# Performance work log

Measured on AMD Instinct MI355X. Metric: run time of the kernel, lower is better.

Reference implementation:

```python
import jax, jax.numpy as jnp
import numpy as np
import math
from jax import lax

B, L, C_IN = 32, 1024, 21
D_MODEL, N_HEADS, D_FF = 512, 8, 2048
E_LAYERS, FACTOR, MA_K = 3, 1, 25
N_CLASSES = 10
EPS = 1e-5


def setup_inputs() -> dict:
    key = jax.random.key(0)
    ks = jax.random.split(key, 12)
    s = 0.02
    return {
        "x_enc": jax.random.normal(ks[0], (B, L, C_IN), jnp.float32),
        "x_mark_enc": jnp.ones((B, L), jnp.float32),
        "conv_emb_w": jax.random.normal(ks[1], (D_MODEL, C_IN, 3), jnp.float32) * s,
        "Wq": jax.random.normal(ks[2], (E_LAYERS, D_MODEL, D_MODEL), jnp.float32) * s,
        "bq": jnp.zeros((E_LAYERS, D_MODEL), jnp.float32),
        "Wk": jax.random.normal(ks[3], (E_LAYERS, D_MODEL, D_MODEL), jnp.float32) * s,
        "bk": jnp.zeros((E_LAYERS, D_MODEL), jnp.float32),
        "Wv": jax.random.normal(ks[4], (E_LAYERS, D_MODEL, D_MODEL), jnp.float32) * s,
        "bv": jnp.zeros((E_LAYERS, D_MODEL), jnp.float32),
        "Wo": jax.random.normal(ks[5], (E_LAYERS, D_MODEL, D_MODEL), jnp.float32) * s,
        "bo": jnp.zeros((E_LAYERS, D_MODEL), jnp.float32),
        "Wff1": jax.random.normal(ks[6], (E_LAYERS, D_FF, D_MODEL), jnp.float32) * s,
        "Wff2": jax.random.normal(ks[7], (E_LAYERS, D_MODEL, D_FF), jnp.float32) * s,
        "ln_g": jnp.ones((D_MODEL,), jnp.float32),
        "ln_b": jnp.zeros((D_MODEL,), jnp.float32),
        "Wproj": jax.random.normal(ks[8], (N_CLASSES, D_MODEL * L), jnp.float32) * 0.001,
        "bproj": jnp.zeros((N_CLASSES,), jnp.float32),
    }


def token_embed(x, w):
    # x: [B, L, C] -> Conv1d(C->D, k=3, circular padding, no bias) -> [B, L, D]
    xp = jnp.pad(x.transpose(0, 2, 1), ((0, 0), (0, 0), (1, 1)), mode='wrap')  # [B,C,L+2]
    y = lax.conv_general_dilated(xp, w, (1,), 'VALID', dimension_numbers=('NCH', 'OIH', 'NCH'))
    return y.transpose(0, 2, 1)


def moving_avg(x, k):
    # replicate-pad then avg-pool with stride 1 (kernel k odd -> same length)
    pad = (k - 1) // 2
    xp = jnp.concatenate([jnp.repeat(x[:, :1], pad, 1), x, jnp.repeat(x[:, -1:], pad, 1)], axis=1)
    return lax.reduce_window(xp, 0.0, lax.add, (1, k, 1), (1, 1, 1), 'VALID') / k


def series_decomp(x, k):
    m = moving_avg(x, k)
    return x - m, m


def auto_correlation(q, k, v):
    # q,k,v: [B, L, H, E]; FFT-based period correlation + time-delay aggregation (inference variant)
    B_, L_, H, E = q.shape
    qf = jnp.fft.rfft(q.transpose(0, 2, 3, 1), axis=-1)   # [B,H,E,Lf]
    kf = jnp.fft.rfft(k.transpose(0, 2, 3, 1), axis=-1)
    corr = jnp.fft.irfft(qf * jnp.conj(kf), n=L_, axis=-1)  # [B,H,E,L]
    values = v.transpose(0, 2, 3, 1)                        # [B,H,E,L]
    mean_value = corr.mean(axis=(1, 2))                     # [B,L]
    top_k = int(FACTOR * math.log(L_))
    weights, delay = lax.top_k(mean_value, top_k)           # [B,k]
    tmp_corr = jax.nn.softmax(weights, axis=-1)
    tmp_values = jnp.concatenate([values, values], axis=-1)  # [B,H,E,2L]
    init_index = jnp.arange(L_)
    agg = jnp.zeros_like(values)
    for i in range(top_k):  # small fixed loop (top_k = 6)
        idx = init_index[None, :] + delay[:, i:i + 1]        # [B,L]
        idx_b = jnp.broadcast_to(idx[:, None, None, :], (B_, H, E, L_))
        pat = jnp.take_along_axis(tmp_values, idx_b, axis=-1)
        agg = agg + pat * tmp_corr[:, i][:, None, None, None]
    return agg.transpose(0, 3, 1, 2)  # [B,L,H,E]


def encoder_layer(x, Wq, bq, Wk, bk, Wv, bv, Wo, bo, Wf1, Wf2):
    B_, L_, D = x.shape
    E = D // N_HEADS
    q = (x @ Wq.T + bq).reshape(B_, L_, N_HEADS, E)
    k = (x @ Wk.T + bk).reshape(B_, L_, N_HEADS, E)
    v = (x @ Wv.T + bv).reshape(B_, L_, N_HEADS, E)
    a = auto_correlation(q, k, v).reshape(B_, L_, D)
    a = a @ Wo.T + bo
    x = x + a
    x, _ = series_decomp(x, MA_K)
    y = jax.nn.gelu(jnp.einsum('bld,fd->blf', x, Wf1), approximate=False)
    y = jnp.einsum('blf,df->bld', y, Wf2)
    res, _ = series_decomp(x + y, MA_K)
    return res


def my_layernorm(x, g, b):
    mu = x.mean(-1, keepdims=True)
    var = ((x - mu) ** 2).mean(-1, keepdims=True)
    xh = (x - mu) / jnp.sqrt(var + EPS) * g + b
    return xh - xh.mean(axis=1, keepdims=True)  # special LN: remove seq-wise mean


def reference(x_enc, x_mark_enc, conv_emb_w, Wq, bq, Wk, bk, Wv, bv, Wo, bo, Wff1, Wff2, ln_g, ln_b, Wproj, bproj):
    x = token_embed(x_enc, conv_emb_w)  # DataEmbedding_wo_pos with x_mark=None
    for l in range(E_LAYERS):
        x = encoder_layer(x, Wq[l], bq[l], Wk[l], bk[l], Wv[l], bv[l], Wo[l], bo[l], Wff1[l], Wff2[l])
    x = my_layernorm(x, ln_g, ln_b)
    out = jax.nn.gelu(x, approximate=False)
    out = out * x_mark_enc[:, :, None]
    out = out.reshape(out.shape[0], -1)
    return out @ Wproj.T + bproj
```

## Files before the change

kernel.cpp:

```cpp
#include <hip/hip_runtime.h>
#include <cstdint>


using u16 = unsigned short;
typedef _Float16 f16x8 __attribute__((ext_vector_type(8)));
typedef float f32x4 __attribute__((ext_vector_type(4)));

#define BB 32
#define LL 1024
#define DD 512
#define DFF 2048

__device__ __forceinline__ float bf2f(u16 u) {
  union { uint32_t i; float f; } v; v.i = ((uint32_t)u) << 16; return v.f;
}
__device__ __forceinline__ u16 f2bf(float f) {
  union { float f; uint32_t i; } v; v.f = f;
  uint32_t r = (v.i + 0x7FFFu + ((v.i >> 16) & 1u)) >> 16;
  return (u16)r;
}
__device__ __forceinline__ float ldi(const void* p, long i, int isf) {
  return isf ? ((const float*)p)[i] : bf2f(((const u16*)p)[i]);
}
__device__ __forceinline__ float gelu_f(float x) {
  return 0.5f * x * (1.0f + erff(x * 0.70710678118654752440f));
}
__device__ __forceinline__ void gld16(const void* g, void* l) {
  __builtin_amdgcn_global_load_lds(
      (const __attribute__((address_space(1))) void*)g,
      (__attribute__((address_space(3))) void*)l, 16, 0, 0);
}

union H8 { f16x8 v; uint4 u; _Float16 h[8]; };
union H4 { uint2 u; _Float16 h[4]; };

__global__ void detect_k(const uint32_t* __restrict__ mark, int* __restrict__ FLAG) {
  if (threadIdx.x == 0) FLAG[0] = (mark[0] == 0x3F800000u) ? 1 : 0;
}

__global__ __launch_bounds__(256) void wT_k(const void* __restrict__ w,
                                            float* __restrict__ wT,
                                            const int* __restrict__ FLAG) {
  const int isf = *FLAG;
  int idx = blockIdx.x * 256 + threadIdx.x;
  if (idx >= 63 * DD) return;
  int c3t = idx / DD;
  int d = idx - c3t * DD;
  wT[idx] = ldi(w, (long)d * 63 + c3t, isf);
}

__global__ __launch_bounds__(256) void conv_embed_k(
    const void* __restrict__ xe, const float* __restrict__ wT,
    float* __restrict__ X, _Float16* __restrict__ XH, _Float16* __restrict__ XL,
    const int* __restrict__ FLAG) {
  const int isf = *FLAG;
  int b = blockIdx.y;
  int l0 = blockIdx.x * 16;
  __shared__ float xs[18][21];
  int tid = threadIdx.x;
  for (int i = tid; i < 18 * 21; i += 256) {
    int r = i / 21, c = i % 21;
    int row = (l0 - 1 + r + LL) & (LL - 1);
    xs[r][c] = ldi(xe, ((long)b * LL + row) * 21 + c, isf);
  }
  __syncthreads();
  for (int d = tid; d < DD; d += 256) {
    float acc[16];
#pragma unroll
    for (int ll = 0; ll < 16; ll++) acc[ll] = 0.0f;
    for (int c = 0; c < 21; c++) {
#pragma unroll
      for (int t = 0; t < 3; t++) {
        float wv = wT[(c * 3 + t) * DD + d];
#pragma unroll
        for (int ll = 0; ll < 16; ll++) acc[ll] += wv * xs[t + ll][c];
      }
    }
    for (int ll = 0; ll < 16; ll++) {
      long idx = ((long)b * LL + l0 + ll) * DD + d;
      float v = acc[ll];
      X[idx] = v;
      _Float16 hv = (_Float16)v;
      XH[idx] = hv;
      XL[idx] = (_Float16)((v - (float)hv) * 512.0f);
    }
  }
}

__global__ __launch_bounds__(256) void tsplit2_k(
    const void* __restrict__ W1, const void* __restrict__ W2, long off,
    _Float16* __restrict__ T1H, _Float16* __restrict__ T1L,
    _Float16* __restrict__ T2H, _Float16* __restrict__ T2L,
    const int* __restrict__ FLAG) {
  const int isf = *FLAG;
  const void* W = blockIdx.z ? W2 : W1;
  _Float16* TH = blockIdx.z ? T2H : T1H;
  _Float16* TL = blockIdx.z ? T2L : T1L;
  __shared__ float t[64][65];
  const int f0 = blockIdx.x * 64, m0 = blockIdx.y * 64;
  const int tid = threadIdx.x;
  const int c = tid & 63, rb = tid >> 6;
#pragma unroll
  for (int r = rb; r < 64; r += 4)
    t[r][c] = ldi(W, off + (long)(f0 + r) * DD + m0 + c, isf);
  __syncthreads();
#pragma unroll
  for (int r = rb; r < 64; r += 4) {
    float v = t[c][r];
    long o = (long)(m0 + r) * DD + f0 + c;
    _Float16 hv = (_Float16)v;
    TH[o] = hv;
    TL[o] = (_Float16)((v - (float)hv) * 512.0f);
  }
}

__global__ __launch_bounds__(256) void split_k(const float* __restrict__ src,
                                               _Float16* __restrict__ dh,
                                               _Float16* __restrict__ dl, int n) {
  long i = ((long)blockIdx.x * 256 + threadIdx.x) * 8;
  if (i >= n) return;
  float4 a = *(const float4*)(src + i);
  float4 b = *(const float4*)(src + i + 4);
  float x[8] = {a.x, a.y, a.z, a.w, b.x, b.y, b.z, b.w};
  H8 h, l;
#pragma unroll
  for (int j = 0; j < 8; j++) {
    _Float16 hv = (_Float16)x[j];
    h.h[j] = hv;
    l.h[j] = (_Float16)((x[j] - (float)hv) * 512.0f);
  }
  *(uint4*)(dh + i) = h.u;
  *(uint4*)(dl + i) = l.u;
}

__global__ __launch_bounds__(256) void acvt_k(const float* __restrict__ src,
                                              _Float16* __restrict__ dst, int n) {
  long i = ((long)blockIdx.x * 256 + threadIdx.x) * 8;
  if (i >= n) return;
  float4 a = *(const float4*)(src + i);
  float4 b = *(const float4*)(src + i + 4);
  H8 r;
  r.h[0] = (_Float16)a.x; r.h[1] = (_Float16)a.y;
  r.h[2] = (_Float16)a.z; r.h[3] = (_Float16)a.w;
  r.h[4] = (_Float16)b.x; r.h[5] = (_Float16)b.y;
  r.h[6] = (_Float16)b.z; r.h[7] = (_Float16)b.w;
  *(uint4*)(dst + i) = r.u;
}

__global__ __launch_bounds__(256) void wcvt6_k(
    const void* __restrict__ Wv, const void* __restrict__ Wo,
    const void* __restrict__ W1, const void* __restrict__ W2,
    long oW, long oF,
    _Float16* __restrict__ Wvh, _Float16* __restrict__ Woh,
    _Float16* __restrict__ W1h, _Float16* __restrict__ W2h,
    const int* __restrict__ FLAG) {
  const int isf = *FLAG;
  long e = ((long)blockIdx.x * 256 + threadIdx.x) * 8;
  const void* src; long soff; _Float16* dst;
  if (e < 262144) { src = Wv; soff = oW + e; dst = Wvh + e; }
  else if (e < 524288) { src = Wo; soff = oW + (e - 262144); dst = Woh + (e - 262144); }
  else if (e < 1572864) { src = W1; soff = oF + (e - 524288); dst = W1h + (e - 524288); }
  else { src = W2; soff = oF + (e - 1572864); dst = W2h + (e - 1572864); }
  H8 r;
  if (isf) {
    const float* s = (const float*)src + soff;
    float4 a = *(const float4*)s;
    float4 b = *(const float4*)(s + 4);
    r.h[0] = (_Float16)a.x; r.h[1] = (_Float16)a.y;
    r.h[2] = (_Float16)a.z; r.h[3] = (_Float16)a.w;
    r.h[4] = (_Float16)b.x; r.h[5] = (_Float16)b.y;
    r.h[6] = (_Float16)b.z; r.h[7] = (_Float16)b.w;
  } else {
    const u16* s = (const u16*)src + soff;
    uint4 u = *(const uint4*)s;
    r.h[0] = (_Float16)bf2f((u16)(u.x & 0xffff));
    r.h[1] = (_Float16)bf2f((u16)(u.x >> 16));
    r.h[2] = (_Float16)bf2f((u16)(u.y & 0xffff));
    r.h[3] = (_Float16)bf2f((u16)(u.y >> 16));
    r.h[4] = (_Float16)bf2f((u16)(u.z & 0xffff));
    r.h[5] = (_Float16)bf2f((u16)(u.z >> 16));
    r.h[6] = (_Float16)bf2f((u16)(u.w & 0xffff));
    r.h[7] = (_Float16)bf2f((u16)(u.w >> 16));
  }
  *(uint4*)(dst) = r.u;
}

__global__ __launch_bounds__(256) void gemm_z(
    const _Float16* __restrict__ Ah, const _Float16* __restrict__ Al,
    const _Float16* __restrict__ Bh, const _Float16* __restrict__ Bl,
    _Float16* __restrict__ Zh, _Float16* __restrict__ Zl,
    int M, int N, int K) {
  __shared__ __align__(16) _Float16 AsH[128 * 32];
  __shared__ __align__(16) _Float16 AsL[128 * 32];
  __shared__ __align__(16) _Float16 BsH[128 * 32];
  __shared__ __align__(16) _Float16 BsL[128 * 32];
  const int n0 = blockIdx.x * 128, m0 = blockIdx.y * 128;
  const int tid = threadIdx.x;
  const int lane = tid & 63, wvi = tid >> 6;
  const int wm = (wvi >> 1) * 64, wn = (wvi & 1) * 64;
  const int l15 = lane & 15, quad = lane >> 4;
  const int ib = wvi * 128 + lane;
  const int r0 = ib >> 2, r1 = r0 + 16;
  const int c0 = ((ib & 3) ^ ((r0 >> 1) & 3)) * 8;
  const int c1 = ((ib & 3) ^ ((r1 >> 1) & 3)) * 8;
  const int lb0 = wvi * 1024, lb1 = wvi * 1024 + 512;
  const long ga0 = (long)(m0 + r0) * K + c0;
  const long ga1 = (long)(m0 + r1) * K + c1;
  const long gb0 = (long)(n0 + r0) * K + c0;
  const long gb1 = (long)(n0 + r1) * K + c1;
  f32x4 aM[4][4], aC[4][4];
#pragma unroll
  for (int i = 0; i < 4; i++)
#pragma unroll
    for (int j = 0; j < 4; j++) {
      aM[i][j] = (f32x4){0.f, 0.f, 0.f, 0.f};
      aC[i][j] = (f32x4){0.f, 0.f, 0.f, 0.f};
    }
  for (int k0 = 0; k0 < K; k0 += 32) {
    __syncthreads();
    gld16(Ah + ga0 + k0, AsH + lb0);
    gld16(Ah + ga1 + k0, AsH + lb1);
    gld16(Al + ga0 + k0, AsL + lb0);
    gld16(Al + ga1 + k0, AsL + lb1);
    gld16(Bh + gb0 + k0, BsH + lb0);
    gld16(Bh + gb1 + k0, BsH + lb1);
    gld16(Bl + gb0 + k0, BsL + lb0);
    gld16(Bl + gb1 + k0, BsL + lb1);
    __syncthreads();
    f16x8 fah[4], fal[4], fbh[4], fbl[4];
#pragma unroll
    for (int mi = 0; mi < 4; mi++) {
      int r = wm + mi * 16 + l15;
      int o = r * 32 + ((quad ^ ((r >> 1) & 3)) * 8);
      fah[mi] = *(const f16x8*)&AsH[o];
      fal[mi] = *(const f16x8*)&AsL[o];
    }
#pragma unroll
    for (int ni = 0; ni < 4; ni++) {
      int r = wn + ni * 16 + l15;
      int o = r * 32 + ((quad ^ ((r >> 1) & 3)) * 8);
      fbh[ni] = *(const f16x8*)&BsH[o];
      fbl[ni] = *(const f16x8*)&BsL[o];
    }
#pragma unroll
    for (int mi = 0; mi < 4; mi++)
#pragma unroll
      for (int ni = 0; ni < 4; ni++) {
        aM[mi][ni] = __builtin_amdgcn_mfma_f32_16x16x32_f16(
            fah[mi], fbh[ni], aM[mi][ni], 0, 0, 0);
        aC[mi][ni] = __builtin_amdgcn_mfma_f32_16x16x32_f16(
            fah[mi], fbl[ni], aC[mi][ni], 0, 0, 0);
        aC[mi][ni] = __builtin_amdgcn_mfma_f32_16x16x32_f16(
            fal[mi], fbh[ni], aC[mi][ni], 0, 0, 0);
      }
  }
#pragma unroll
  for (int mi = 0; mi < 4; mi++) {
    int rowg = m0 + wm + mi * 16 + quad * 4;
#pragma unroll
    for (int ni = 0; ni < 4; ni++) {
      int colg = n0 + wn + ni * 16 + l15;
#pragma unroll
      for (int rr = 0; rr < 4; rr++) {
        long off = (long)(rowg + rr) * N + colg;
        float z = aM[mi][ni][rr] + aC[mi][ni][rr] * (1.0f / 512.0f);
        _Float16 zh = (_Float16)z;
        Zh[off] = zh;
        Zl[off] = (_Float16)((z - (float)zh) * 512.0f);
      }
    }
  }
}

__global__ __launch_bounds__(256) void qkmv_hl(
    const _Float16* __restrict__ Zh, const _Float16* __restrict__ Zl,
    const _Float16* __restrict__ Xh, const _Float16* __restrict__ Xl,
    float* __restrict__ MV) {
  __shared__ __align__(16) _Float16 AsH[128 * 32];
  __shared__ __align__(16) _Float16 AsL[128 * 32];
  __shared__ __align__(16) _Float16 BsH[128 * 32];
  __shared__ __align__(16) _Float16 BsL[128 * 32];
  __shared__ float diag[255];
  const int bz = blockIdx.z;
  const long bb = (long)bz * LL * DD;
  const int n0 = blockIdx.x * 128, m0 = blockIdx.y * 128;
  const int tid = threadIdx.x;
  const int lane = tid & 63, wvi = tid >> 6;
  const int wm = (wvi >> 1) * 64, wn = (wvi & 1) * 64;
  const int l15 = lane & 15, quad = lane >> 4;
  const int ib = wvi * 128 + lane;
  const int r0 = ib >> 2, r1 = r0 + 16;
  const int c0 = ((ib & 3) ^ ((r0 >> 1) & 3)) * 8;
  const int c1 = ((ib & 3) ^ ((r1 >> 1) & 3)) * 8;
  const int lb0 = wvi * 1024, lb1 = wvi * 1024 + 512;
  const long ga0 = bb + (long)(m0 + r0) * DD + c0;
  const long ga1 = bb + (long)(m0 + r1) * DD + c1;
  const long gb0 = bb + (long)(n0 + r0) * DD + c0;
  const long gb1 = bb + (long)(n0 + r1) * DD + c1;
  if (tid < 255) diag[tid] = 0.0f;
  f32x4 aM[4][4], aC[4][4];
#pragma unroll
  for (int i = 0; i < 4; i++)
#pragma unroll
    for (int j = 0; j < 4; j++) {
      aM[i][j] = (f32x4){0.f, 0.f, 0.f, 0.f};
      aC[i][j] = (f32x4){0.f, 0.f, 0.f, 0.f};
    }
  for (int k0 = 0; k0 < DD; k0 += 32) {
    __syncthreads();
    gld16(Zh + ga0 + k0, AsH + lb0);
    gld16(Zh + ga1 + k0, AsH + lb1);
    gld16(Zl + ga0 + k0, AsL + lb0);
    gld16(Zl + ga1 + k0, AsL + lb1);
    gld16(Xh + gb0 + k0, BsH + lb0);
    gld16(Xh + gb1 + k0, BsH + lb1);
    gld16(Xl + gb0 + k0, BsL + lb0);
    gld16(Xl + gb1 + k0, BsL + lb1);
    __syncthreads();
    f16x8 fah[4], fal[4], fbh[4], fbl[4];
#pragma unroll
    for (int mi = 0; mi < 4; mi++) {
      int r = wm + mi * 16 + l15;
      int o = r * 32 + ((quad ^ ((r >> 1) & 3)) * 8);
      fah[mi] = *(const f16x8*)&AsH[o];
      fal[mi] = *(const f16x8*)&AsL[o];
    }
#pragma unroll
    for (int ni = 0; ni < 4; ni++) {
      int r = wn + ni * 16 + l15;
      int o = r * 32 + ((quad ^ ((r >> 1) & 3)) * 8);
      fbh[ni] = *(const f16x8*)&BsH[o];
      fbl[ni] = *(const f16x8*)&BsL[o];
    }
#pragma unroll
    for (int mi = 0; mi < 4; mi++)
#pragma unroll
      for (int ni = 0; ni < 4; ni++) {
        aM[mi][ni] = __builtin_amdgcn_mfma_f32_16x16x32_f16(
            fah[mi], fbh[ni], aM[mi][ni], 0, 0, 0);
        aC[mi][ni] = __builtin_amdgcn_mfma_f32_16x16x32_f16(
            fah[mi], fbl[ni], aC[mi][ni], 0, 0, 0);
        aC[mi][ni] = __builtin_amdgcn_mfma_f32_16x16x32_f16(
            fal[mi], fbh[ni], aC[mi][ni], 0, 0, 0);
      }
  }
#pragma unroll
  for (int g = -3; g <= 3; g++) {
#pragma unroll
    for (int rr = 0; rr < 4; rr++) {
      float s = 0.0f;
#pragma unroll
      for (int mi = 0; mi < 4; mi++) {
        int ni = mi - g;
        if (ni >= 0 && ni < 4)
          s += aM[mi][ni][rr] + aC[mi][ni][rr] * (1.0f / 512.0f);
      }
      int d = 127 + (wm - wn) + g * 16 + quad * 4 + rr - l15;
      atomicAdd(&diag[d], s);
    }
  }
  __syncthreads();
  if (tid < 255) {
    int tau = (m0 - n0 + tid - 127 + LL) & (LL - 1);
    atomicAdd(&MV[(long)bz * LL + tau], diag[tid] * (1.0f / 512.0f));
  }
}

template <int FLAGS>
__global__ __launch_bounds__(256) void gemm_h(
    const _Float16* __restrict__ A, const _Float16* __restrict__ W,
    const void* __restrict__ biasBase, long bOff,
    const float* __restrict__ R, void* __restrict__ Cout,
    int M, int N, int K, const int* __restrict__ FLAG) {
  constexpr bool HAS_BIAS = (FLAGS & 1) != 0;
  constexpr bool DO_GELU = (FLAGS & 2) != 0;
  constexpr bool DO_RES = (FLAGS & 4) != 0;
  constexpr bool OUT_H = (FLAGS & 8) != 0;
  __shared__ __align__(16) _Float16 As[128 * 64];
  __shared__ __align__(16) _Float16 Bs[128 * 64];
  const int n0 = blockIdx.x * 128, m0 = blockIdx.y * 128;
  const int tid = threadIdx.x;
  const int lane = tid & 63, wvi = tid >> 6;
  const int wm = (wvi >> 1) * 64, wn = (wvi & 1) * 64;
  const int l15 = lane & 15, quad = lane >> 4;
  const _Float16* gA[4];
  const _Float16* gB[4];
  int ldsOff[4];
#pragma unroll
  for (int j = 0; j < 4; j++) {
    int ib = wvi * 256 + j * 64 + lane;
    int row = ib >> 3, p = ib & 7;
    int gc = ((p & 4) | ((p & 3) ^ ((row >> 1) & 3))) * 8;
    gA[j] = A + (long)(m0 + row) * K + gc;
    gB[j] = W + (long)(n0 + row) * K + gc;
    ldsOff[j] = wvi * 2048 + j * 512;
  }
  f32x4 acc[4][4];
#pragma unroll
  for (int i = 0; i < 4; i++)
#pragma unroll
    for (int j = 0; j < 4; j++) acc[i][j] = (f32x4){0.f, 0.f, 0.f, 0.f};
  for (int k0 = 0; k0 < K; k0 += 64) {
    __syncthreads();
#pragma unroll
    for (int j = 0; j < 4; j++) gld16(gA[j] + k0, As + ldsOff[j]);
#pragma unroll
    for (int j = 0; j < 4; j++) gld16(gB[j] + k0, Bs + ldsOff[j]);
    __syncthreads();
#pragma unroll
    for (int ks = 0; ks < 2; ks++) {
      f16x8 af[4], bfr[4];
#pragma unroll
      for (int mi = 0; mi < 4; mi++) {
        int r = wm + mi * 16 + l15;
        af[mi] = *(const f16x8*)&As[r * 64 + (ks * 4 + (quad ^ ((r >> 1) & 3))) * 8];
      }
#pragma unroll
      for (int ni = 0; ni < 4; ni++) {
        int r = wn + ni * 16 + l15;
        bfr[ni] = *(const f16x8*)&Bs[r * 64 + (ks * 4 + (quad ^ ((r >> 1) & 3))) * 8];
      }
#pragma unroll
      for (int mi = 0; mi < 4; mi++)
#pragma unroll
        for (int ni = 0; ni < 4; ni++)
          acc[mi][ni] = __builtin_amdgcn_mfma_f32_16x16x32_f16(
              af[mi], bfr[ni], acc[mi][ni], 0, 0, 0);
    }
  }
  float bcol[4];
  if constexpr (HAS_BIAS) {
    const int isf = *FLAG;
#pragma unroll
    for (int ni = 0; ni < 4; ni++)
      bcol[ni] = ldi(biasBase, bOff + n0 + wn + ni * 16 + l15, isf);
  }
#pragma unroll
  for (int mi = 0; mi < 4; mi++) {
    int rowg = m0 + wm + mi * 16 + quad * 4;
#pragma unroll
    for (int ni = 0; ni < 4; ni++) {
      int colg = n0 + wn + ni * 16 + l15;
#pragma unroll
      for (int rr = 0; rr < 4; rr++) {
        long off = (long)(rowg + rr) * N + colg;
        float v = acc[mi][ni][rr];
        if constexpr (HAS_BIAS) v += bcol[ni];
        if constexpr (DO_RES) v += R[off];
        if constexpr (DO_GELU) v = gelu_f(v);
        if constexpr (OUT_H) ((_Float16*)Cout)[off] = (_Float16)v;
        else ((float*)Cout)[off] = v;
      }
    }
  }
}

__global__ __launch_bounds__(256) void topk_k(const float* __restrict__ MV,
                                              float* __restrict__ WGT,
                                              int* __restrict__ DLY) {
  int b = blockIdx.x;
  __shared__ float vals[LL];
  __shared__ float rv[256];
  __shared__ int ri[256];
  __shared__ float selv[6];
  int tid = threadIdx.x;
  for (int i = tid; i < LL; i += 256) vals[i] = MV[(long)b * LL + i];
  __syncthreads();
  for (int it = 0; it < 6; it++) {
    float bv = -1e30f;
    int bi = LL - 1;
    for (int i = tid; i < LL; i += 256) {
      float v = vals[i];
      if (v > bv || (v == bv && i < bi)) { bv = v; bi = i; }
    }
    rv[tid] = bv; ri[tid] = bi;
    __syncthreads();
    for (int st = 128; st > 0; st >>= 1) {
      if (tid < st) {
        float ov = rv[tid + st]; int oi = ri[tid + st];
        if (ov > rv[tid] || (ov == rv[tid] && oi < ri[tid])) {
          rv[tid] = ov; ri[tid] = oi;
        }
      }
      __syncthreads();
    }
    if (tid == 0) {
      selv[it] = rv[0];
      DLY[b * 6 + it] = ri[0];
      vals[ri[0]] = -1e30f;
    }
    __syncthreads();
  }
  if (tid == 0) {
    float mx = selv[0];
    float e[6], s = 0.0f;
    for (int i = 0; i < 6; i++) { e[i] = expf(selv[i] - mx); s += e[i]; }
    for (int i = 0; i < 6; i++) WGT[b * 6 + i] = e[i] / s;
  }
}

__global__ __launch_bounds__(128) void agg_k(const _Float16* __restrict__ V,
                                             const float* __restrict__ WGT,
                                             const int* __restrict__ DLY,
                                             _Float16* __restrict__ O) {
  int l = blockIdx.x, b = blockIdx.y;
  int tid = threadIdx.x;
  float w[6]; int dl[6];
#pragma unroll
  for (int i = 0; i < 6; i++) { w[i] = WGT[b * 6 + i]; dl[i] = DLY[b * 6 + i]; }
  long base = (long)b * LL * DD;
  int d = tid * 4;
  float a0 = 0, a1 = 0, a2 = 0, a3 = 0;
#pragma unroll
  for (int i = 0; i < 6; i++) {
    int row = (l + dl[i]) & (LL - 1);
    H4 t; t.u = *(const uint2*)&V[base + (long)row * DD + d];
    a0 += w[i] * (float)t.h[0];
    a1 += w[i] * (float)t.h[1];
    a2 += w[i] * (float)t.h[2];
    a3 += w[i] * (float)t.h[3];
  }
  H4 r;
  r.h[0] = (_Float16)a0; r.h[1] = (_Float16)a1;
  r.h[2] = (_Float16)a2; r.h[3] = (_Float16)a3;
  *(uint2*)&O[base + (long)l * DD + d] = r.u;
}

__global__ __launch_bounds__(256) void decomp_k(const float* __restrict__ Xin,
                                                float* __restrict__ Out) {
  int d = blockIdx.x * 256 + threadIdx.x;
  int l0 = blockIdx.y * 64;
  int b = blockIdx.z;
  const float* xb = Xin + (long)b * LL * DD + d;
  float* ob = Out + (long)b * LL * DD + d;
  float wsum = 0.0f;
  for (int j = l0 - 12; j <= l0 + 12; j++) {
    int jj = min(max(j, 0), LL - 1);
    wsum += xb[(long)jj * DD];
  }
  for (int l = l0; l < l0 + 64; l++) {
    float xv = xb[(long)l * DD];
    ob[(long)l * DD] = xv - wsum * (1.0f / 25.0f);
    int ja = min(l + 13, LL - 1);
    int jr = max(l - 12, 0);
    wsum += xb[(long)ja * DD] - xb[(long)jr * DD];
  }
}

__global__ __launch_bounds__(256) void ln_k(const float* __restrict__ X,
                                            const void* __restrict__ g,
                                            const void* __restrict__ be,
                                            float* __restrict__ XHo,
                                            const int* __restrict__ FLAG) {
  const int isf = *FLAG;
  int l = blockIdx.x, b = blockIdx.y;
  const float* xr = X + ((long)b * LL + l) * DD;
  int tid = threadIdx.x;
  float x0 = xr[tid], x1 = xr[tid + 256];
  __shared__ float rs[256], rq[256];
  rs[tid] = x0 + x1;
  rq[tid] = x0 * x0 + x1 * x1;
  __syncthreads();
  for (int st = 128; st > 0; st >>= 1) {
    if (tid < st) { rs[tid] += rs[tid + st]; rq[tid] += rq[tid + st]; }
    __syncthreads();
  }
  float mu = rs[0] * (1.0f / 512.0f);
  float var = rq[0] * (1.0f / 512.0f) - mu * mu;
  float rstd = rsqrtf(var + 1e-5f);
  float* o = XHo + ((long)b * LL + l) * DD;
  o[tid] = (x0 - mu) * rstd * ldi(g, tid, isf) + ldi(be, tid, isf);
  o[tid + 256] = (x1 - mu) * rstd * ldi(g, tid + 256, isf) + ldi(be, tid + 256, isf);
}

__global__ __launch_bounds__(256) void colmean_k(const float* __restrict__ XHo,
                                                 float* __restrict__ CM) {
  int d = blockIdx.x * 256 + threadIdx.x;
  int b = blockIdx.y;
  const float* p = XHo + (long)b * LL * DD + d;
  float s = 0.0f;
  for (int l = 0; l < LL; l++) s += p[(long)l * DD];
  CM[(long)b * DD + d] = s * (1.0f / 1024.0f);
}

__global__ __launch_bounds__(256) void geluout_k(const float* __restrict__ XHo,
                                                 const float* __restrict__ CM,
                                                 const void* __restrict__ mark,
                                                 float* __restrict__ OUT,
                                                 const int* __restrict__ FLAG) {
  const int isf = *FLAG;
  int l = blockIdx.x, b = blockIdx.y;
  int tid = threadIdx.x;
  float mk = ldi(mark, (long)b * LL + l, isf);
  long off = ((long)b * LL + l) * DD;
#pragma unroll
  for (int h = 0; h < 2; h++) {
    int d = tid + h * 256;
    float v = XHo[off + d] - CM[(long)b * DD + d];
    OUT[off + d] = gelu_f(v) * mk;
  }
}

__global__ __launch_bounds__(256) void proj1_k(const float* __restrict__ OUT,
                                               const void* __restrict__ Wp,
                                               float* __restrict__ PB,
                                               const int* __restrict__ FLAG) {
  const int isf = *FLAG;
  int chunk = blockIdx.x, n = blockIdx.y, b = blockIdx.z;
  long e0 = (long)chunk * 32768;
  const float* xb = OUT + (long)b * 524288 + e0;
  long wbase = (long)n * 524288 + e0;
  int tid = threadIdx.x;
  float s = 0.0f;
  if (isf) {
    const float* wr = (const float*)Wp + wbase;
    for (int i = tid * 4; i < 32768; i += 1024) {
      float4 x = *(const float4*)&xb[i];
      float4 w = *(const float4*)&wr[i];
      s += x.x * w.x + x.y * w.y + x.z * w.z + x.w * w.w;
    }
  } else {
    const u16* wr = (const u16*)Wp + wbase;
    for (int i = tid * 4; i < 32768; i += 1024) {
      float4 x = *(const float4*)&xb[i];
      uint2 u = *(const uint2*)&wr[i];
      s += x.x * bf2f((u16)(u.x & 0xffff)) + x.y * bf2f((u16)(u.x >> 16)) +
           x.z * bf2f((u16)(u.y & 0xffff)) + x.w * bf2f((u16)(u.y >> 16));
    }
  }
  __shared__ float red[256];
  red[tid] = s;
  __syncthreads();
  for (int st = 128; st > 0; st >>= 1) {
    if (tid < st) red[tid] += red[tid + st];
    __syncthreads();
  }
  if (tid == 0) PB[((long)b * 10 + n) * 16 + chunk] = red[0];
}

__global__ __launch_bounds__(320) void proj2_k(const float* __restrict__ PB,
                                               const void* __restrict__ bp,
                                               void* __restrict__ out,
                                               const int* __restrict__ FLAG) {
  const int isf = *FLAG;
  int id = threadIdx.x;
  int b = id / 10, n = id % 10;
  float s = ldi(bp, n, isf);
  for (int c = 0; c < 16; c++) s += PB[((long)b * 10 + n) * 16 + c];
  if (isf) ((float*)out)[b * 10 + n] = s;
  else ((u16*)out)[b * 10 + n] = f2bf(s);
}

extern "C" void kernel_launch(void* const* d_in, const int* in_sizes, int n_in,
                              void* d_out, int out_size, void* d_ws, size_t ws_size,
                              hipStream_t stream) {
  const void* xe = d_in[0];
  const void* mark = d_in[1];
  const void* cw = d_in[2];
  const void* Wq = d_in[3];
  const void* Wk = d_in[5];
  const void* Wv = d_in[7];
  const void* bv = d_in[8];
  const void* Wo = d_in[9];
  const void* bo = d_in[10];
  const void* Wff1 = d_in[11];
  const void* Wff2 = d_in[12];
  const void* lng = d_in[13];
  const void* lnb = d_in[14];
  const void* Wp = d_in[15];
  const void* bp = d_in[16];

  char* ws = (char*)d_ws;
  float* X      = (float*)(ws + 0L);
  _Float16* XH  = (_Float16*)(ws + 67108864L);
  _Float16* XL  = (_Float16*)(ws + 100663296L);
  _Float16* AGh = (_Float16*)(ws + 100663296L);
  _Float16* ZH  = (_Float16*)(ws + 134217728L);
  _Float16* ZL  = (_Float16*)(ws + 138412032L);
  _Float16* Ph  = (_Float16*)(ws + 134217728L);
  float* wT     = (float*)(ws + 142606336L);
  _Float16* KTH = (_Float16*)(ws + 142606336L);
  _Float16* KTL = (_Float16*)(ws + 143130624L);
  _Float16* QTH = (_Float16*)(ws + 143654912L);
  _Float16* QTL = (_Float16*)(ws + 144179200L);
  _Float16* GH  = (_Float16*)(ws + 144703488L);
  _Float16* GL  = (_Float16*)(ws + 145227776L);
  _Float16* Wvh = (_Float16*)(ws + 142606336L);
  _Float16* Woh = (_Float16*)(ws + 143130624L);
  _Float16* W1h = (_Float16*)(ws + 143654912L);
  _Float16* W2h = (_Float16*)(ws + 145752064L);
  float* MV  = (float*)(ws + 147849216L);
  float* WGT = (float*)(ws + 147980288L);
  int*   DLY = (int*)(ws + 147981312L);
  float* CM  = (float*)(ws + 147982336L);
  float* PB  = (float*)(ws + 148047872L);
  int*  FLAG = (int*)(ws + 148068352L);
  float* S2  = (float*)(ws + 67108864L);
  _Float16* Hb = (_Float16*)X;

  const long AD = (long)LL * DD;
  const int M = BB * LL;

  detect_k<<<1, 64, 0, stream>>>((const uint32_t*)mark, FLAG);
  wT_k<<<126, 256, 0, stream>>>(cw, wT, FLAG);
  conv_embed_k<<<dim3(64, 32), 256, 0, stream>>>(xe, wT, X, XH, XL, FLAG);

  for (int l = 0; l < 3; l++) {
    const long oW = (long)l * DD * DD;
    const long oB = (long)l * DD;
    const long oF = (long)l * DFF * DD;

    tsplit2_k<<<dim3(8, 8, 2), 256, 0, stream>>>(Wk, Wq, oW,
                                                 KTH, KTL, QTH, QTL, FLAG);
    gemm_z<<<dim3(4, 4), 256, 0, stream>>>(KTH, KTL, QTH, QTL,
                                           GH, GL, 512, 512, 512);
    hipMemsetAsync(MV, 0, (long)BB * LL * sizeof(float), stream);
    for (int cb = 0; cb < 8; cb++) {
      const long co = (long)cb * 4 * AD;
      gemm_z<<<dim3(4, 32), 256, 0, stream>>>(
          XH + co, XL + co, GH, GL, ZH, ZL, 4096, DD, DD);
      qkmv_hl<<<dim3(8, 8, 4), 256, 0, stream>>>(
          ZH, ZL, XH + co, XL + co, MV + (long)cb * 4 * LL);
    }
    topk_k<<<32, 256, 0, stream>>>(MV, WGT, DLY);

    wcvt6_k<<<1280, 256, 0, stream>>>(Wv, Wo, Wff1, Wff2, oW, oF,
                                      Wvh, Woh, W1h, W2h, FLAG);

    for (int cb = 0; cb < 4; cb++) {
      const _Float16* xh = XH + (long)cb * 8 * AD;
      gemm_h<1 | 8><<<dim3(4, 64), 256, 0, stream>>>(
          xh, Wvh, bv, oB, nullptr, Ph, 8192, DD, DD, FLAG);
      agg_k<<<dim3(1024, 8), 128, 0, stream>>>(
          Ph, WGT + cb * 48, DLY + cb * 48, AGh + (long)cb * 8 * AD);
    }

    gemm_h<1 | 4><<<dim3(4, 256), 256, 0, stream>>>(
        AGh, Woh, bo, oB, X, X, M, DD, DD, FLAG);

    decomp_k<<<dim3(2, 16, 32), 256, 0, stream>>>(X, S2);

    for (int cb = 0; cb < 4; cb++) {
      float* xd = S2 + (long)cb * 8 * AD;
      acvt_k<<<2048, 256, 0, stream>>>(xd, Ph, 4194304);
      gemm_h<2 | 8><<<dim3(16, 64), 256, 0, stream>>>(
          Ph, W1h, nullptr, 0, nullptr, Hb, 8192, DFF, DD, FLAG);
      gemm_h<4><<<dim3(4, 64), 256, 0, stream>>>(
          Hb, W2h, nullptr, 0, xd, xd, 8192, DD, DFF, FLAG);
    }

    decomp_k<<<dim3(2, 16, 32), 256, 0, stream>>>(S2, X);
    if (l < 2) split_k<<<8192, 256, 0, stream>>>(X, XH, XL, 16777216);
  }

  ln_k<<<dim3(1024, 32), 256, 0, stream>>>(X, lng, lnb, S2, FLAG);
  colmean_k<<<dim3(2, 32), 256, 0, stream>>>(S2, CM);
  geluout_k<<<dim3(1024, 32), 256, 0, stream>>>(S2, CM, mark, X, FLAG);
  proj1_k<<<dim3(16, 10, 32), 256, 0, stream>>>(X, Wp, PB, FLAG);
  proj2_k<<<1, 320, 0, stream>>>(PB, bp, d_out, FLAG);
}
```

Measured before the change: 3.640 ms.

## Split column-mean into partial sums and restructure projection for weight reuse across batch

The column-mean kernel now runs on 8x more blocks, each summing 128 rows into partial sums, and geluout combines the 8 partials itself. The final projection is restructured so each block loads its slice of all 10 class weights into registers once and reuses them across all 32 batch rows. Wave shuffles and shared memory do the reduction, and a second kernel sums the 512 per-block partials. This cuts the 32x re-reading of the large projection weight and raises parallelism in the low-occupancy colmean step, at the cost of more partial-sum traffic and register pressure from the 40 weight values per thread.

Result: no change. 3.593 ms (-1.3%).

```diff
diff --git a/kernel.cpp b/kernel.cpp
--- a/kernel.cpp
+++ b/kernel.cpp
@@ -574,17 +574,18 @@
 }
 
 __global__ __launch_bounds__(256) void colmean_k(const float* __restrict__ XHo,
-                                                 float* __restrict__ CM) {
+                                                 float* __restrict__ CMp) {
   int d = blockIdx.x * 256 + threadIdx.x;
-  int b = blockIdx.y;
-  const float* p = XHo + (long)b * LL * DD + d;
+  int part = blockIdx.y;
+  int b = blockIdx.z;
+  const float* p = XHo + (long)b * LL * DD + (long)part * 128 * DD + d;
   float s = 0.0f;
-  for (int l = 0; l < LL; l++) s += p[(long)l * DD];
-  CM[(long)b * DD + d] = s * (1.0f / 1024.0f);
+  for (int l = 0; l < 128; l++) s += p[(long)l * DD];
+  CMp[((long)part * BB + b) * DD + d] = s;
 }
 
 __global__ __launch_bounds__(256) void geluout_k(const float* __restrict__ XHo,
-                                                 const float* __restrict__ CM,
+                                                 const float* __restrict__ CMp,
                                                  const void* __restrict__ mark,
                                                  float* __restrict__ OUT,
                                                  const int* __restrict__ FLAG) {
@@ -596,59 +597,90 @@
 #pragma unroll
   for (int h = 0; h < 2; h++) {
     int d = tid + h * 256;
-    float v = XHo[off + d] - CM[(long)b * DD + d];
+    float cs = 0.0f;
+#pragma unroll
+    for (int p = 0; p < 8; p++) cs += CMp[((long)p * BB + b) * DD + d];
+    float v = XHo[off + d] - cs * (1.0f / 1024.0f);
     OUT[off + d] = gelu_f(v) * mk;
   }
 }
 
 __global__ __launch_bounds__(256) void proj1_k(const float* __restrict__ OUT,
                                                const void* __restrict__ Wp,
-                                               float* __restrict__ PB,
+                                               float* __restrict__ PB2,
                                                const int* __restrict__ FLAG) {
   const int isf = *FLAG;
-  int chunk = blockIdx.x, n = blockIdx.y, b = blockIdx.z;
-  long e0 = (long)chunk * 32768;
-  const float* xb = OUT + (long)b * 524288 + e0;
-  long wbase = (long)n * 524288 + e0;
+  const int blk = blockIdx.x;
+  const int tid = threadIdx.x;
+  const int wave = tid >> 6, lane = tid & 63;
+  const int grp = lane >> 4, ln = lane & 15;
+  const long e = (long)blk * 1024 + tid * 4;
+  float w[10][4];
+  if (isf) {
+    const float* wp = (const float*)Wp;
+#pragma unroll
+    for (int n = 0; n < 10; n++) {
+      float4 t = *(const float4*)&wp[(long)n * 524288 + e];
+      w[n][0] = t.x; w[n][1] = t.y; w[n][2] = t.z; w[n][3] = t.w;
+    }
+  } else {
+    const u16* wp = (const u16*)Wp;
+#pragma unroll
+    for (int n = 0; n < 10; n++) {
+      uint2 u = *(const uint2*)&wp[(long)n * 524288 + e];
+      w[n][0] = bf2f((u16)(u.x & 0xffff));
+      w[n][1] = bf2f((u16)(u.x >> 16));
+      w[n][2] = bf2f((u16)(u.y & 0xffff));
+      w[n][3] = bf2f((u16)(u.y >> 16));
+    }
+  }
+  __shared__ float sm[4][4][BB][16];
+  float4 xn = *(const float4*)&OUT[e];
+  for (int b = 0; b < BB; b++) {
+    float4 x = xn;
+    if (b < BB - 1) xn = *(const float4*)&OUT[(long)(b + 1) * 524288 + e];
+    float acc[10];
+#pragma unroll
+    for (int n = 0; n < 10; n++)
+      acc[n] = x.x * w[n][0] + x.y * w[n][1] + x.z * w[n][2] + x.w * w[n][3];
+#pragma unroll
+    for (int s = 1; s <= 8; s <<= 1)
+#pragma unroll
+      for (int n = 0; n < 10; n++) acc[n] += __shfl_xor(acc[n], s, 64);
+    float v = 0.0f;
+#pragma unroll
+    for (int n = 0; n < 10; n++) v = (ln == n) ? acc[n] : v;
+    if (ln < 10) sm[wave][grp][b][ln] = v;
+  }
+  __syncthreads();
+  for (int o = tid; o < BB * 10; o += 256) {
+    int b = o / 10, n = o - b * 10;
+    float s = 0.0f;
+#pragma unroll
+    for (int w4 = 0; w4 < 4; w4++)
+#pragma unroll
+      for (int g = 0; g < 4; g++) s += sm[w4][g][b][n];
+    PB2[(long)o * 512 + blk] = s;
+  }
+}
+
+__global__ __launch_bounds__(64) void proj2_k(const float* __restrict__ PB2,
+                                              const void* __restrict__ bp,
+                                              void* __restrict__ out,
+                                              const int* __restrict__ FLAG) {
+  const int isf = *FLAG;
+  int n = blockIdx.x, b = blockIdx.y;
+  int o = b * 10 + n;
   int tid = threadIdx.x;
   float s = 0.0f;
-  if (isf) {
-    const float* wr = (const float*)Wp + wbase;
-    for (int i = tid * 4; i < 32768; i += 1024) {
-      float4 x = *(const float4*)&xb[i];
-      float4 w = *(const float4*)&wr[i];
-      s += x.x * w.x + x.y * w.y + x.z * w.z + x.w * w.w;
-    }
-  } else {
-    const u16* wr = (const u16*)Wp + wbase;
-    for (int i = tid * 4; i < 32768; i += 1024) {
-      float4 x = *(const float4*)&xb[i];
-      uint2 u = *(const uint2*)&wr[i];
-      s += x.x * bf2f((u16)(u.x & 0xffff)) + x.y * bf2f((u16)(u.x >> 16)) +
-           x.z * bf2f((u16)(u.y & 0xffff)) + x.w * bf2f((u16)(u.y >> 16));
-    }
-  }
-  __shared__ float red[256];
-  red[tid] = s;
-  __syncthreads();
-  for (int st = 128; st > 0; st >>= 1) {
-    if (tid < st) red[tid] += red[tid + st];
-    __syncthreads();
-  }
-  if (tid == 0) PB[((long)b * 10 + n) * 16 + chunk] = red[0];
-}
-
-__global__ __launch_bounds__(320) void proj2_k(const float* __restrict__ PB,
-                                               const void* __restrict__ bp,
-                                               void* __restrict__ out,
-                                               const int* __restrict__ FLAG) {
-  const int isf = *FLAG;
-  int id = threadIdx.x;
-  int b = id / 10, n = id % 10;
-  float s = ldi(bp, n, isf);
-  for (int c = 0; c < 16; c++) s += PB[((long)b * 10 + n) * 16 + c];
-  if (isf) ((float*)out)[b * 10 + n] = s;
-  else ((u16*)out)[b * 10 + n] = f2bf(s);
+  for (int j = tid; j < 512; j += 64) s += PB2[(long)o * 512 + j];
+#pragma unroll
+  for (int st = 32; st > 0; st >>= 1) s += __shfl_xor(s, st, 64);
+  if (tid == 0) {
+    s += ldi(bp, n, isf);
+    if (isf) ((float*)out)[o] = s;
+    else ((u16*)out)[o] = f2bf(s);
+  }
 }
 
 extern "C" void kernel_launch(void* const* d_in, const int* in_sizes, int n_in,
@@ -678,6 +710,7 @@
   _Float16* ZH  = (_Float16*)(ws + 134217728L);
   _Float16* ZL  = (_Float16*)(ws + 138412032L);
   _Float16* Ph  = (_Float16*)(ws + 134217728L);
+  float* CMp    = (float*)(ws + 134217728L);
   float* wT     = (float*)(ws + 142606336L);
   _Float16* KTH = (_Float16*)(ws + 142606336L);
   _Float16* KTL = (_Float16*)(ws + 143130624L);
@@ -692,10 +725,9 @@
   float* MV  = (float*)(ws + 147849216L);
   float* WGT = (float*)(ws + 147980288L);
   int*   DLY = (int*)(ws + 147981312L);
-  float* CM  = (float*)(ws + 147982336L);
-  float* PB  = (float*)(ws + 148047872L);
   int*  FLAG = (int*)(ws + 148068352L);
   float* S2  = (float*)(ws + 67108864L);
+  float* PB2 = (float*)(ws + 67108864L);
   _Float16* Hb = (_Float16*)X;
 
   const long AD = (long)LL * DD;
@@ -754,8 +786,8 @@
   }
 
   ln_k<<<dim3(1024, 32), 256, 0, stream>>>(X, lng, lnb, S2, FLAG);
-  colmean_k<<<dim3(2, 32), 256, 0, stream>>>(S2, CM);
-  geluout_k<<<dim3(1024, 32), 256, 0, stream>>>(S2, CM, mark, X, FLAG);
-  proj1_k<<<dim3(16, 10, 32), 256, 0, stream>>>(X, Wp, PB, FLAG);
-  proj2_k<<<1, 320, 0, stream>>>(PB, bp, d_out, FLAG);
-}
+  colmean_k<<<dim3(2, 8, 32), 256, 0, stream>>>(S2, CMp);
+  geluout_k<<<dim3(1024, 32), 256, 0, stream>>>(S2, CMp, mark, X, FLAG);
+  proj1_k<<<512, 256, 0, stream>>>(X, Wp, PB2, FLAG);
+  proj2_k<<<dim3(10, 32), 64, 0, stream>>>(PB2, bp, d_out, FLAG);
+}
```
